# Kernel optimization log

Measured on AMD Instinct MI355X. Metric: run time of the kernel, lower is better.

## Reference

```python
import jax, jax.numpy as jnp
import numpy as np

I, H, NH, A = 128, 2048, 2, 4   # input_size, hidden_size, n_hidden, alpha_dim
K = 2 * A * A                   # per-position theta entries
B = 8192


def make_masks():
    # MADE sequential-ordering masks, identical to DART.create_masks
    inp = np.arange(I)
    degrees = [inp] + [np.arange(H) % (I - 1) for _ in range(NH + 1)] + [np.arange(I) - 1]
    masks = [(d1[:, None] >= d0[None, :]).astype(np.float32)
             for d0, d1 in zip(degrees[:-1], degrees[1:])]
    # last mask repeated per theta entry: repeat(1, K).view(-1, H) == row-repeat
    masks[-1] = np.repeat(masks[-1], K, axis=0)
    return [jnp.asarray(m) for m in masks]


def setup_inputs() -> dict:
    key = jax.random.key(0)
    ks = jax.random.split(key, 5)
    x = jax.random.normal(ks[0], (B, I), dtype=jnp.float32)

    def lin(k, out_dim, in_dim):
        kw, kb = jax.random.split(k)
        s = 1.0 / np.sqrt(in_dim)
        W = jax.random.uniform(kw, (out_dim, in_dim), minval=-s, maxval=s, dtype=jnp.float32)
        b = jax.random.uniform(kb, (out_dim,), minval=-s, maxval=s, dtype=jnp.float32)
        return W, b

    W0, b0 = lin(ks[1], H, I)
    W1, b1 = lin(ks[2], H, H)
    W2, b2 = lin(ks[3], H, H)
    W3, b3 = lin(ks[4], I * K, H)
    return dict(x=x, W0=W0, b0=b0, W1=W1, b1=b1, W2=W2, b2=b2, W3=W3, b3=b3)


def logexpmm(a, b):
    # log-domain matmul: out[..., i, j] = logsumexp_k(a[..., i, k] + b[..., k, j])
    return jax.nn.logsumexp(a[..., :, :, None] + b[..., None, :, :], axis=-2)


def reference(x, W0, b0, W1, b1, W2, b2, W3, b3):
    m = make_masks()
    h = jax.nn.relu(x @ (m[0] * W0).T + b0)
    h = jax.nn.relu(h @ (m[1] * W1).T + b1)
    h = jax.nn.relu(h @ (m[2] * W2).T + b2)
    theta = (h @ (m[3] * W3).T + b3).reshape(-1, I, 2, A, A)
    mu, alpha = theta[:, :, 0], theta[:, :, 1]  # (B, I, A, A)

    LOG2PI = float(np.log(2.0 * np.pi))
    xe = x[:, :, None, None]
    # Normal(mu, exp(alpha)).log_prob(x) - log(alpha_dim)
    logp = (-0.5 * ((xe - mu) * jnp.exp(-alpha)) ** 2
            - alpha - 0.5 * LOG2PI - jnp.log(jnp.float32(A)))

    first = logp[:, 0, 0:1]        # (B, 1, A)
    last = logp[:, -1, :, 0:1]     # (B, A, 1)
    inner = jnp.swapaxes(logp[:, 1:-1], 0, 1)  # (I-2, B, A, A)

    def step(carry, mtx):
        return logexpmm(carry, mtx), None

    prod, _ = jax.lax.scan(step, inner[0], inner[1:])
    return logexpmm(first, logexpmm(prod, last))  # (B, 1, 1)
```

## Files before the change

kernel.cpp:

```cpp
#include <hip/hip_runtime.h>
#include <hip/hip_bf16.h>
#include <cstdint>
#include <cstddef>

#define AS1 __attribute__((address_space(1)))
#define AS3 __attribute__((address_space(3)))

typedef __bf16 bf16x8  __attribute__((ext_vector_type(8)));
typedef float  floatx4 __attribute__((ext_vector_type(4)));

__device__ __forceinline__ void load_lds16(const void* g, void* l) {
    __builtin_amdgcn_global_load_lds((AS1 void*)g, (AS3 void*)l, 16, 0, 0);
}

__device__ __forceinline__ float fexp2(float x) { return __builtin_amdgcn_exp2f(x); }
__device__ __forceinline__ float flog2(float x) { return __builtin_amdgcn_logf(x); }

#define LOG2E 1.4426950408889634f
#define LN2   0.6931471805599453f
#define C0K   2.3052328943245633f

__device__ __forceinline__ float logp2(float xv, float mu, float al) {
    float e = fexp2(-al * LOG2E);
    float z = (xv - mu) * e;
    return (-0.5f * z * z - al - C0K) * LOG2E;
}
__device__ __forceinline__ float lse4(float a0, float a1, float a2, float a3) {
    float mx = fmaxf(fmaxf(a0, a1), fmaxf(a2, a3));
    return mx + flog2(fexp2(a0 - mx) + fexp2(a1 - mx) +
                      fexp2(a2 - mx) + fexp2(a3 - mx));
}
__device__ __forceinline__ void lmm4(const float* Aa, const float* Bb, float* D) {
#pragma unroll
    for (int r = 0; r < 4; ++r)
#pragma unroll
        for (int c = 0; c < 4; ++c)
            D[r * 4 + c] = lse4(Aa[r * 4 + 0] + Bb[0 * 4 + c],
                                Aa[r * 4 + 1] + Bb[1 * 4 + c],
                                Aa[r * 4 + 2] + Bb[2 * 4 + c],
                                Aa[r * 4 + 3] + Bb[3 * 4 + c]);
}

__device__ __forceinline__ int resp_s(int p) {
    return p < 272 ? p / 17 : 16 + ((p - 272) >> 4);
}
__device__ __forceinline__ int invp_s(int p) {
    if (p < 272) { int d = p / 17; int r = p - d * 17;
                   return r < 16 ? d + r * 127 : 2032 + d; }
    int d = 16 + ((p - 272) >> 4); int j = (p - 272) & 15;
    return d + j * 127;
}
__device__ __forceinline__ int cnt_le(int D) {
    return D < 16 ? (D + 1) * 17 : 272 + ((D - 15) << 4);
}

__global__ __launch_bounds__(256)
void prep_all(const float* __restrict__ x,  const float* __restrict__ W0,
              const float* __restrict__ W1, const float* __restrict__ W2,
              const float* __restrict__ W3,
              __bf16* __restrict__ xb,  __bf16* __restrict__ w0m,
              __bf16* __restrict__ w1m, __bf16* __restrict__ w2m,
              __bf16* __restrict__ w3m)
{
    __shared__ float lds[2048];
    const int blk = blockIdx.x;
    const int tid = threadIdx.x;
    const int t8  = tid * 8;

    if (blk < 640) {
        bf16x8 o;
        if (blk < 512) {
            size_t base = (size_t)blk * 2048 + t8;
            floatx4 a = *(const floatx4*)(x + base);
            floatx4 b = *(const floatx4*)(x + base + 4);
#pragma unroll
            for (int j = 0; j < 4; ++j) { o[j] = (__bf16)a[j]; o[4 + j] = (__bf16)b[j]; }
            *(bf16x8*)(xb + base) = o;
        } else {
            long idx = (long)(blk - 512) * 2048 + t8;
            int p_n = (int)(idx >> 7);
            int c   = (int)(idx & 127);
            int dg  = resp_s(p_n);
            const float* s = W0 + (long)invp_s(p_n) * 128 + c;
            floatx4 a = *(const floatx4*)s;
            floatx4 b = *(const floatx4*)(s + 4);
#pragma unroll
            for (int j = 0; j < 8; ++j) {
                float v = j < 4 ? a[j] : b[j - 4];
                o[j] = (__bf16)((dg >= c + j) ? v : 0.0f);
            }
            *(bf16x8*)(w0m + idx) = o;
        }
        return;
    }

    const float* srow; __bf16* drow; int deg_n; bool strict;
    if (blk < 2688) {
        int p_n = blk - 640;
        srow = W1 + (size_t)invp_s(p_n) * 2048; drow = w1m + (size_t)p_n * 2048;
        deg_n = resp_s(p_n); strict = false;
    } else if (blk < 4736) {
        int p_n = blk - 2688;
        srow = W2 + (size_t)invp_s(p_n) * 2048; drow = w2m + (size_t)p_n * 2048;
        deg_n = resp_s(p_n); strict = false;
    } else {
        int n = blk - 4736;
        srow = W3 + (size_t)n * 2048; drow = w3m + (size_t)n * 2048;
        deg_n = n >> 5; strict = true;
    }
    floatx4 a = *(const floatx4*)(srow + t8);
    floatx4 b = *(const floatx4*)(srow + t8 + 4);
    *(floatx4*)&lds[t8]     = a;
    *(floatx4*)&lds[t8 + 4] = b;
    __syncthreads();
    bf16x8 o;
#pragma unroll
    for (int j = 0; j < 8; ++j) {
        int p = t8 + j;
        float v = lds[invp_s(p)];
        int dg = resp_s(p);
        bool keep = strict ? (deg_n > dg) : (deg_n >= dg);
        o[j] = (__bf16)(keep ? v : 0.0f);
    }
    *(bf16x8*)(drow + t8) = o;
}

template <bool RELU, bool OBF16, bool TLAYOUT, bool PERMBIAS, int LMODE>
__global__ __launch_bounds__(256, 4)
void gemm_bt(const __bf16* __restrict__ A, const __bf16* __restrict__ Bw,
             const float* __restrict__ bias, void* __restrict__ Cout,
             int N, int K)
{
    __shared__ __align__(16) __bf16 lsA[128 * 64];
    __shared__ __align__(16) __bf16 lsB[128 * 64];
    const int tid  = threadIdx.x;
    const int wave = tid >> 6;
    const int lane = tid & 63;
    const int bm = blockIdx.x;
    const int bn = (gridDim.y - 1) - blockIdx.y;
    const int wm = wave >> 1, wn = wave & 1;

    const int r8 = lane >> 3;
    const int cb = (lane & 7) ^ r8;
    const __bf16* gsrc[8];
    __bf16* ldst[8];
#pragma unroll
    for (int t = 0; t < 8; ++t) {
        int j = wave * 8 + t;
        if (j < 16) {
            int row = bm * 128 + j * 8 + r8;
            gsrc[t] = A + (size_t)row * K + cb * 8;
            ldst[t] = lsA + j * 512;
        } else {
            int jj = j - 16;
            int row = bn * 128 + jj * 8 + r8;
            gsrc[t] = Bw + (size_t)row * K + cb * 8;
            ldst[t] = lsB + jj * 512;
        }
    }

    const int fr  = lane & 15;
    const int ks  = lane >> 4;
    const int sx  = fr & 7;
    const int sl0 = ((ks)     ^ sx) * 8;
    const int sl1 = ((4 + ks) ^ sx) * 8;
    const __bf16* arow[4];
    const __bf16* brow[4];
#pragma unroll
    for (int i = 0; i < 4; ++i) {
        arow[i] = lsA + (wm * 64 + i * 16 + fr) * 64;
        brow[i] = lsB + (wn * 64 + i * 16 + fr) * 64;
    }

    floatx4 acc[4][4];
    const floatx4 vzero = {0.f, 0.f, 0.f, 0.f};
#pragma unroll
    for (int mi = 0; mi < 4; ++mi)
#pragma unroll
        for (int ni = 0; ni < 4; ++ni) acc[mi][ni] = vzero;

    const int nk = K >> 6;
    int limit;
    if (LMODE == 0)      limit = (cnt_le(resp_s(bn * 128 + 127)) + 63) >> 6;
    else if (LMODE == 1) { int D = 4 * bn + 2; if (D > 126) D = 126;
                           limit = (cnt_le(D) + 63) >> 6; }
    else                 limit = (resp_s(bn * 128 + 127) + 64) >> 6;
    if (limit > nk) limit = nk;

    for (int it = 0; it < limit; ++it) {
        const int kt = it << 6;
        __syncthreads();
#pragma unroll
        for (int t = 0; t < 8; ++t)
            load_lds16((const void*)(gsrc[t] + kt), (void*)ldst[t]);
        __syncthreads();
        bf16x8 af[4], bf[4];
#pragma unroll
        for (int i = 0; i < 4; ++i) af[i] = *(const bf16x8*)(arow[i] + sl0);
#pragma unroll
        for (int i = 0; i < 4; ++i) bf[i] = *(const bf16x8*)(brow[i] + sl0);
#pragma unroll
        for (int mi = 0; mi < 4; ++mi)
#pragma unroll
            for (int ni = 0; ni < 4; ++ni)
                acc[mi][ni] = __builtin_amdgcn_mfma_f32_16x16x32_bf16(
                    af[mi], bf[ni], acc[mi][ni], 0, 0, 0);
#pragma unroll
        for (int i = 0; i < 4; ++i) af[i] = *(const bf16x8*)(arow[i] + sl1);
#pragma unroll
        for (int i = 0; i < 4; ++i) bf[i] = *(const bf16x8*)(brow[i] + sl1);
#pragma unroll
        for (int mi = 0; mi < 4; ++mi)
#pragma unroll
            for (int ni = 0; ni < 4; ++ni)
                acc[mi][ni] = __builtin_amdgcn_mfma_f32_16x16x32_bf16(
                    af[mi], bf[ni], acc[mi][ni], 0, 0, 0);
    }

    const int cn  = lane & 15;
    const int cr4 = (lane >> 4) * 4;
#pragma unroll
    for (int ni = 0; ni < 4; ++ni) {
        int col = bn * 128 + wn * 64 + ni * 16 + cn;
        float bv = bias[PERMBIAS ? invp_s(col) : col];
#pragma unroll
        for (int mi = 0; mi < 4; ++mi) {
            int row0 = bm * 128 + wm * 64 + mi * 16 + cr4;
#pragma unroll
            for (int q = 0; q < 4; ++q) {
                float v = acc[mi][ni][q] + bv;
                if (RELU) v = fmaxf(v, 0.f);
                if (TLAYOUT) {
                    size_t addr = (size_t)(bm * 2 + wm) * ((size_t)N * 64)
                                + (size_t)col * 64 + (mi * 16 + cr4 + q);
                    ((__bf16*)Cout)[addr] = (__bf16)v;
                } else if (OBF16) {
                    ((__bf16*)Cout)[(size_t)(row0 + q) * N + col] = (__bf16)v;
                } else {
                    ((float*)Cout)[(size_t)(row0 + q) * N + col] = v;
                }
            }
        }
    }
}

#define CFENCE() asm volatile("" ::: "memory")
#define BARX()  do { CFENCE(); __builtin_amdgcn_s_barrier(); CFENCE(); } while (0)
#define WVM2()  asm volatile("s_waitcnt vmcnt(2)" ::: "memory")
#define WVM0()  asm volatile("s_waitcnt vmcnt(0)" ::: "memory")
#define WLGK()  asm volatile("s_waitcnt lgkmcnt(0)" ::: "memory")

template <bool RELU, bool OBF16, bool TLAYOUT, bool PERMBIAS, int LMODE>
__global__ __launch_bounds__(512)
void gemm8p(const __bf16* __restrict__ A, const __bf16* __restrict__ Bw,
            const float* __restrict__ bias, void* __restrict__ Cout,
            int N, int K)
{
    __shared__ __align__(16) __bf16 ls[2 * 24576];
    const int tid  = threadIdx.x;
    const int wave = tid >> 6;
    const int lane = tid & 63;
    const int bm = blockIdx.x;
    const int bn = (gridDim.y - 1) - blockIdx.y;
    const int wm = wave >> 1, wn = wave & 1;

    const int l8 = lane >> 3;
    const int cb = (lane & 7) ^ l8;
    const __bf16* gA[2][2];  int dA[2][2];
    const __bf16* gB[2];     int dB[2];
#pragma unroll
    for (int h = 0; h < 2; ++h)
#pragma unroll
        for (int s = 0; s < 2; ++s) {
            int rt = h * 128 + wave * 16 + s * 8;
            gA[h][s] = A + (size_t)(bm * 256 + rt + l8) * K + cb * 8;
            dA[h][s] = rt * 64;
        }
#pragma unroll
    for (int s = 0; s < 2; ++s) {
        int rt = wave * 16 + s * 8;
        gB[s] = Bw + (size_t)(bn * 128 + rt + l8) * K + cb * 8;
        dB[s] = 16384 + rt * 64;
    }

#define STG_A(buf, kt) do { \
    load_lds16((const void*)(gA[0][0] + (kt)), (void*)(ls + (buf)*24576 + dA[0][0])); \
    load_lds16((const void*)(gA[0][1] + (kt)), (void*)(ls + (buf)*24576 + dA[0][1])); \
    load_lds16((const void*)(gA[1][0] + (kt)), (void*)(ls + (buf)*24576 + dA[1][0])); \
    load_lds16((const void*)(gA[1][1] + (kt)), (void*)(ls + (buf)*24576 + dA[1][1])); } while (0)
#define STG_B(buf, kt) do { \
    load_lds16((const void*)(gB[0] + (kt)), (void*)(ls + (buf)*24576 + dB[0])); \
    load_lds16((const void*)(gB[1] + (kt)), (void*)(ls + (buf)*24576 + dB[1])); } while (0)

    const int fr  = lane & 15;
    const int ks  = lane >> 4;
    const int sx  = fr & 7;
    const int sl0 = ((ks)     ^ sx) * 8;
    const int sl1 = ((4 + ks) ^ sx) * 8;
    int aoff[4], boff[4];
#pragma unroll
    for (int i = 0; i < 4; ++i) {
        aoff[i] = (wm * 64 + i * 16 + fr) * 64;
        boff[i] = 16384 + (wn * 64 + i * 16 + fr) * 64;
    }

    floatx4 acc[4][4];
    const floatx4 vzero = {0.f, 0.f, 0.f, 0.f};
#pragma unroll
    for (int mi = 0; mi < 4; ++mi)
#pragma unroll
        for (int ni = 0; ni < 4; ++ni) acc[mi][ni] = vzero;

    bf16x8 bfr[4][2], afr[2][2];

#define DSRD_B(buf) do { \
    _Pragma("unroll") \
    for (int ni = 0; ni < 4; ++ni) { \
        bfr[ni][0] = *(const bf16x8*)(ls + (buf)*24576 + boff[ni] + sl0); \
        bfr[ni][1] = *(const bf16x8*)(ls + (buf)*24576 + boff[ni] + sl1); } } while (0)
#define DSRD_A(buf, q) do { \
    _Pragma("unroll") \
    for (int j = 0; j < 2; ++j) { \
        afr[j][0] = *(const bf16x8*)(ls + (buf)*24576 + aoff[2*(q)+j] + sl0); \
        afr[j][1] = *(const bf16x8*)(ls + (buf)*24576 + aoff[2*(q)+j] + sl1); } } while (0)
#define MFMA16(q) do { \
    __builtin_amdgcn_s_setprio(1); \
    _Pragma("unroll") \
    for (int j = 0; j < 2; ++j) \
    _Pragma("unroll") \
    for (int ni = 0; ni < 4; ++ni) { \
        acc[2*(q)+j][ni] = __builtin_amdgcn_mfma_f32_16x16x32_bf16( \
            afr[j][0], bfr[ni][0], acc[2*(q)+j][ni], 0, 0, 0); \
        acc[2*(q)+j][ni] = __builtin_amdgcn_mfma_f32_16x16x32_bf16( \
            afr[j][1], bfr[ni][1], acc[2*(q)+j][ni], 0, 0, 0); } \
    __builtin_amdgcn_s_setprio(0); } while (0)

    const int nk = K >> 6;
    int limit;
    if (LMODE == 0)      limit = (cnt_le(resp_s(bn * 128 + 127)) + 63) >> 6;
    else if (LMODE == 1) { int D = 4 * bn + 2; if (D > 126) D = 126;
                           limit = (cnt_le(D) + 63) >> 6; }
    else                 limit = (resp_s(bn * 128 + 127) + 64) >> 6;
    if (limit > nk) limit = nk;
    const int NT = limit;

    STG_B(0, 0);
    STG_A(0, 0);
    if (NT > 1) { STG_B(1, 64); WVM2(); } else { WVM0(); }
    BARX();

    for (int t = 0; ; t += 2) {
        const int kt1 = (t + 1) << 6, kt2 = (t + 2) << 6, kt3 = (t + 3) << 6;
        const bool has1 = t + 1 < NT, has2 = t + 2 < NT, has3 = t + 3 < NT;

        DSRD_B(0);
        DSRD_A(0, 0);
        if (has1) STG_A(1, kt1);
        BARX(); WLGK();
        MFMA16(0);
        BARX();

        DSRD_A(0, 1);
        if (has2) STG_B(0, kt2);
        BARX(); WLGK();
        MFMA16(1);
        if (!has1) break;
        if (has2) WVM2(); else WVM0();
        BARX();

        DSRD_B(1);
        DSRD_A(1, 0);
        if (has2) STG_A(0, kt2);
        BARX(); WLGK();
        MFMA16(0);
        BARX();

        DSRD_A(1, 1);
        if (has3) STG_B(1, kt3);
        BARX(); WLGK();
        MFMA16(1);
        if (!has2) break;
        if (has3) WVM2(); else WVM0();
        BARX();
    }

    const int cn  = lane & 15;
    const int cr4 = (lane >> 4) * 4;
#pragma unroll
    for (int ni = 0; ni < 4; ++ni) {
        int col = bn * 128 + wn * 64 + ni * 16 + cn;
        float bv = bias[PERMBIAS ? invp_s(col) : col];
#pragma unroll
        for (int mi = 0; mi < 4; ++mi) {
            int row0 = bm * 256 + wm * 64 + mi * 16 + cr4;
#pragma unroll
            for (int q = 0; q < 4; ++q) {
                float v = acc[mi][ni][q] + bv;
                if (RELU) v = fmaxf(v, 0.f);
                if (TLAYOUT) {
                    size_t addr = (size_t)(bm * 4 + wm) * ((size_t)N * 64)
                                + (size_t)col * 64 + (mi * 16 + cr4 + q);
                    ((__bf16*)Cout)[addr] = (__bf16)v;
                } else if (OBF16) {
                    ((__bf16*)Cout)[(size_t)(row0 + q) * N + col] = (__bf16)v;
                } else {
                    ((float*)Cout)[(size_t)(row0 + q) * N + col] = v;
                }
            }
        }
    }
#undef STG_A
#undef STG_B
#undef DSRD_B
#undef DSRD_A
#undef MFMA16
}

__global__ __launch_bounds__(448)
void chain_all(const __bf16* __restrict__ th2,
               const float* __restrict__ x,
               float* __restrict__ out)
{
    __shared__ float xs[32 * 129];
    __shared__ float Pl[32 * 238];
    const int tid = threadIdx.x;
    const int blk = blockIdx.x;

    for (int idx = tid; idx < 4096; idx += 448) {
        int bl = idx >> 7, i = idx & 127;
        xs[bl * 129 + i] = x[(size_t)blk * 4096 + idx];
    }
    __syncthreads();

    const int s  = tid >> 5;
    const int bl = tid & 31;
    const int b64 = (blk & 1) * 32 + bl;
    const __bf16* tb = th2 + (size_t)(blk >> 1) * (4096 * 64) + b64;

    {
        const int i0 = 1 + s * 9;
        const __bf16* tp = tb + (size_t)i0 * 32 * 64;
        float M[4][4];
#pragma unroll
        for (int r = 0; r < 4; ++r)
#pragma unroll
            for (int c = 0; c < 4; ++c) M[r][c] = (r == c) ? 0.f : -1e30f;

        for (int ii = 0; ii < 9; ++ii) {
            float mu[16], al[16];
#pragma unroll
            for (int j = 0; j < 16; ++j) mu[j] = (float)tp[(size_t)j * 64];
#pragma unroll
            for (int j = 0; j < 16; ++j) al[j] = (float)tp[(size_t)(16 + j) * 64];
            float xv = xs[bl * 129 + i0 + ii];
            tp += 2048;
            float lp[16];
#pragma unroll
            for (int j = 0; j < 16; ++j) lp[j] = logp2(xv, mu[j], al[j]);
            float Mn[4][4];
#pragma unroll
            for (int r = 0; r < 4; ++r)
#pragma unroll
                for (int c = 0; c < 4; ++c)
                    Mn[r][c] = lse4(M[r][0] + lp[0 + c], M[r][1] + lp[4 + c],
                                    M[r][2] + lp[8 + c], M[r][3] + lp[12 + c]);
#pragma unroll
            for (int r = 0; r < 4; ++r)
#pragma unroll
                for (int c = 0; c < 4; ++c) M[r][c] = Mn[r][c];
        }
        float* pb = Pl + bl * 238 + s * 17;
#pragma unroll
        for (int r = 0; r < 4; ++r)
#pragma unroll
            for (int c = 0; c < 4; ++c) pb[r * 4 + c] = M[r][c];
    }
    __syncthreads();

    float Q[16];
    if (tid < 224) {
        const float* base = Pl + bl * 238;
        lmm4(base + (2 * s) * 17, base + (2 * s + 1) * 17, Q);
    }
    __syncthreads();
    if (tid < 224) {
        float* dst = Pl + bl * 238 + s * 17;
#pragma unroll
        for (int e = 0; e < 16; ++e) dst[e] = Q[e];
    }
    __syncthreads();

    if (tid < 32) {
        const float* base = Pl + tid * 238;
        float M[16], T[16];
#pragma unroll
        for (int e = 0; e < 16; ++e) M[e] = base[e];
#pragma unroll
        for (int j = 1; j < 7; ++j) {
            lmm4(M, base + j * 17, T);
#pragma unroll
            for (int e = 0; e < 16; ++e) M[e] = T[e];
        }
        const int bb64 = (blk & 1) * 32 + tid;
        const __bf16* tbb = th2 + (size_t)(blk >> 1) * (4096 * 64) + bb64;
        float x0 = xs[tid * 129 + 0];
        float xl = xs[tid * 129 + 127];
        float last[4], t4[4], f4[4];
#pragma unroll
        for (int c = 0; c < 4; ++c)
            last[c] = logp2(xl, (float)tbb[(size_t)(4064 + c * 4) * 64],
                                (float)tbb[(size_t)(4064 + 16 + c * 4) * 64]);
#pragma unroll
        for (int r = 0; r < 4; ++r)
            t4[r] = lse4(M[r * 4 + 0] + last[0], M[r * 4 + 1] + last[1],
                         M[r * 4 + 2] + last[2], M[r * 4 + 3] + last[3]);
#pragma unroll
        for (int r = 0; r < 4; ++r)
            f4[r] = logp2(x0, (float)tbb[(size_t)r * 64],
                              (float)tbb[(size_t)(16 + r) * 64]);
        out[blk * 32 + tid] = LN2 * lse4(f4[0] + t4[0], f4[1] + t4[1],
                                         f4[2] + t4[2], f4[3] + t4[3]);
    }
}

extern "C" void kernel_launch(void* const* d_in, const int* in_sizes, int n_in,
                              void* d_out, int out_size, void* d_ws, size_t ws_size,
                              hipStream_t stream)
{
    (void)in_sizes; (void)n_in; (void)out_size; (void)ws_size;
    const float* x  = (const float*)d_in[0];
    const float* W0 = (const float*)d_in[1];
    const float* b0 = (const float*)d_in[2];
    const float* W1 = (const float*)d_in[3];
    const float* b1 = (const float*)d_in[4];
    const float* W2 = (const float*)d_in[5];
    const float* b2 = (const float*)d_in[6];
    const float* W3 = (const float*)d_in[7];
    const float* b3 = (const float*)d_in[8];

    char* ws = (char*)d_ws;
    const size_t MB = 1024 * 1024;
    __bf16* h2  = (__bf16*)(ws + 0);
    __bf16* xb  = (__bf16*)(ws + 32 * MB);
    __bf16* w0m = (__bf16*)(ws + 34 * MB);
    __bf16* w1m = (__bf16*)(ws + 35 * MB);
    __bf16* w2m = (__bf16*)(ws + 43 * MB);
    __bf16* th  = (__bf16*)(ws + 0);
    __bf16* w3m = (__bf16*)(ws + 64 * MB);
    __bf16* h1  = (__bf16*)(ws + 80 * MB);
    __bf16* h3  = h1;

    prep_all<<<8832, 256, 0, stream>>>(x, W0, W1, W2, W3, xb, w0m, w1m, w2m, w3m);

    gemm_bt<true, true, false, true, 2><<<dim3(64, 16), 256, 0, stream>>>(
        xb, w0m, b0, h1, 2048, 128);
    gemm8p<true, true, false, true, 0><<<dim3(32, 16), 512, 0, stream>>>(
        h1, w1m, b1, h2, 2048, 2048);
    gemm8p<true, true, false, true, 0><<<dim3(32, 16), 512, 0, stream>>>(
        h2, w2m, b2, h3, 2048, 2048);
    gemm8p<false, false, true, false, 1><<<dim3(32, 32), 512, 0, stream>>>(
        h3, w3m, b3, th, 4096, 2048);

    chain_all<<<256, 448, 0, stream>>>(th, x, (float*)d_out);
}
```

Measured before the change: 322.0 us.

## Use 256x256-tile GEMM kernel for final masked projection layer

Adds a new GEMM kernel with 256x256 output tiles per 512-thread block, using double-buffered global-to-LDS loads, finer interleaving of LDS reads with MFMA in half-tiles, and partial vmcnt waits. The final W3 projection now runs on it with half as many blocks. Larger tiles raise arithmetic intensity and cut global traffic per FLOP, but they also mean fewer blocks and more register and LDS pressure, which lowers occupancy. They also make the masked-K limit per tile coarser.

```diff
diff --git a/kernel.cpp b/kernel.cpp
--- a/kernel.cpp
+++ b/kernel.cpp
@@ -246,6 +246,7 @@
 
 #define CFENCE() asm volatile("" ::: "memory")
 #define BARX()  do { CFENCE(); __builtin_amdgcn_s_barrier(); CFENCE(); } while (0)
+#define WVM6()  asm volatile("s_waitcnt vmcnt(6)" ::: "memory")
 #define WVM2()  asm volatile("s_waitcnt vmcnt(2)" ::: "memory")
 #define WVM0()  asm volatile("s_waitcnt vmcnt(0)" ::: "memory")
 #define WLGK()  asm volatile("s_waitcnt lgkmcnt(0)" ::: "memory")
@@ -416,6 +417,194 @@
 #undef MFMA16
 }
 
+template <bool RELU, bool OBF16, bool TLAYOUT, bool PERMBIAS, int LMODE>
+__global__ __launch_bounds__(512)
+void gemm256(const __bf16* __restrict__ A, const __bf16* __restrict__ Bw,
+             const float* __restrict__ bias, void* __restrict__ Cout,
+             int N, int K)
+{
+    __shared__ __align__(16) __bf16 ls[2 * 32768];
+    const int tid  = threadIdx.x;
+    const int wave = tid >> 6;
+    const int lane = tid & 63;
+    const int bm = blockIdx.x;
+    const int bn = (gridDim.y - 1) - blockIdx.y;
+    const int wm = wave >> 2, wn = wave & 3;
+
+    const int l8 = lane >> 3;
+    const int cb = (lane & 7) ^ l8;
+    const __bf16* gA[2][2]; int lA[2][2];
+    const __bf16* gB[2][2]; int lB[2][2];
+#pragma unroll
+    for (int h = 0; h < 2; ++h)
+#pragma unroll
+        for (int c = 0; c < 2; ++c) {
+            int rA = ((wave & 4) ? 128 : 0) + h * 64 + (wave & 3) * 16 + c * 8;
+            gA[h][c] = A + (size_t)(bm * 256 + rA + l8) * K + cb * 8;
+            lA[h][c] = (rA + l8) * 64 + (lane & 7) * 8;
+            int rB = (wave >> 1) * 64 + h * 32 + (wave & 1) * 16 + c * 8;
+            gB[h][c] = Bw + (size_t)(bn * 256 + rB + l8) * K + cb * 8;
+            lB[h][c] = 16384 + (rB + l8) * 64 + (lane & 7) * 8;
+        }
+
+#define STG_AU(h, buf, kt) do { \
+    load_lds16((const void*)(gA[h][0] + (kt)), (void*)(ls + (buf)*32768 + lA[h][0])); \
+    load_lds16((const void*)(gA[h][1] + (kt)), (void*)(ls + (buf)*32768 + lA[h][1])); } while (0)
+#define STG_BU(h, buf, kt) do { \
+    load_lds16((const void*)(gB[h][0] + (kt)), (void*)(ls + (buf)*32768 + lB[h][0])); \
+    load_lds16((const void*)(gB[h][1] + (kt)), (void*)(ls + (buf)*32768 + lB[h][1])); } while (0)
+
+    const int fr  = lane & 15;
+    const int ks  = lane >> 4;
+    const int sx  = fr & 7;
+    const int sl0 = ((ks)     ^ sx) * 8;
+    const int sl1 = ((4 + ks) ^ sx) * 8;
+    int aof[2][4], bof[2][2];
+#pragma unroll
+    for (int h = 0; h < 2; ++h) {
+#pragma unroll
+        for (int m = 0; m < 4; ++m)
+            aof[h][m] = (wm * 128 + h * 64 + m * 16 + fr) * 64;
+#pragma unroll
+        for (int n = 0; n < 2; ++n)
+            bof[h][n] = 16384 + (wn * 64 + h * 32 + n * 16 + fr) * 64;
+    }
+
+    bf16x8 af[4][2], b0[2][2], b1[2][2];
+    floatx4 acc[8][4];
+    const floatx4 vzero = {0.f, 0.f, 0.f, 0.f};
+#pragma unroll
+    for (int mi = 0; mi < 8; ++mi)
+#pragma unroll
+        for (int ni = 0; ni < 4; ++ni) acc[mi][ni] = vzero;
+
+#define DSRD_A2(buf, mh) do { _Pragma("unroll") \
+    for (int m = 0; m < 4; ++m) { \
+        af[m][0] = *(const bf16x8*)(ls + (buf)*32768 + aof[mh][m] + sl0); \
+        af[m][1] = *(const bf16x8*)(ls + (buf)*32768 + aof[mh][m] + sl1); } } while (0)
+#define DSRD_B0(buf) do { _Pragma("unroll") \
+    for (int n = 0; n < 2; ++n) { \
+        b0[n][0] = *(const bf16x8*)(ls + (buf)*32768 + bof[0][n] + sl0); \
+        b0[n][1] = *(const bf16x8*)(ls + (buf)*32768 + bof[0][n] + sl1); } } while (0)
+#define DSRD_B1(buf) do { _Pragma("unroll") \
+    for (int n = 0; n < 2; ++n) { \
+        b1[n][0] = *(const bf16x8*)(ls + (buf)*32768 + bof[1][n] + sl0); \
+        b1[n][1] = *(const bf16x8*)(ls + (buf)*32768 + bof[1][n] + sl1); } } while (0)
+#define MF16(mh, BF, nh) do { \
+    __builtin_amdgcn_s_setprio(1); \
+    _Pragma("unroll") \
+    for (int m = 0; m < 4; ++m) \
+    _Pragma("unroll") \
+    for (int n = 0; n < 2; ++n) { \
+        acc[(mh)*4+m][(nh)*2+n] = __builtin_amdgcn_mfma_f32_16x16x32_bf16( \
+            af[m][0], BF[n][0], acc[(mh)*4+m][(nh)*2+n], 0, 0, 0); \
+        acc[(mh)*4+m][(nh)*2+n] = __builtin_amdgcn_mfma_f32_16x16x32_bf16( \
+            af[m][1], BF[n][1], acc[(mh)*4+m][(nh)*2+n], 0, 0, 0); } \
+    __builtin_amdgcn_s_setprio(0); } while (0)
+
+    const int nk = K >> 6;
+    int limit;
+    if (LMODE == 0)      limit = (cnt_le(resp_s(bn * 256 + 255)) + 63) >> 6;
+    else if (LMODE == 1) { int D = 8 * bn + 6; if (D > 126) D = 126;
+                           limit = (cnt_le(D) + 63) >> 6; }
+    else                 limit = (resp_s(bn * 256 + 255) + 64) >> 6;
+    if (limit > nk) limit = nk;
+    const int NT = limit;
+
+    STG_AU(0, 0, 0); STG_BU(0, 0, 0); STG_BU(1, 0, 0); STG_AU(1, 0, 0);
+    if (NT > 1) { STG_AU(0, 1, 64); STG_BU(0, 1, 64); STG_BU(1, 1, 64); WVM6(); }
+    else        { WVM0(); }
+    BARX();
+
+    int t = 0;
+    for (; t + 1 < NT; t += 2) {
+        const int kt1 = (t + 1) << 6, kt2 = (t + 2) << 6, kt3 = (t + 3) << 6;
+        const bool st2 = (t + 2 < NT), st3 = (t + 3 < NT);
+
+        DSRD_A2(0, 0); DSRD_B0(0);
+        STG_AU(1, 1, kt1);
+        BARX(); WLGK();
+        MF16(0, b0, 0);
+        BARX();
+        DSRD_B1(0);
+        if (st2) STG_AU(0, 0, kt2);
+        BARX(); WLGK();
+        MF16(0, b1, 1);
+        BARX();
+        DSRD_A2(0, 1);
+        if (st2) STG_BU(0, 0, kt2);
+        BARX(); WLGK();
+        MF16(1, b1, 1);
+        BARX();
+        if (st2) STG_BU(1, 0, kt2);
+        BARX();
+        MF16(1, b0, 0);
+        if (st2) WVM6(); else WVM0();
+        BARX();
+        DSRD_A2(1, 0); DSRD_B0(1);
+        if (st2) STG_AU(1, 0, kt2);
+        BARX(); WLGK();
+        MF16(0, b0, 0);
+        BARX();
+        DSRD_B1(1);
+        if (st3) STG_AU(0, 1, kt3);
+        BARX(); WLGK();
+        MF16(0, b1, 1);
+        BARX();
+        DSRD_A2(1, 1);
+        if (st3) STG_BU(0, 1, kt3);
+        BARX(); WLGK();
+        MF16(1, b1, 1);
+        BARX();
+        if (st3) STG_BU(1, 1, kt3);
+        BARX();
+        MF16(1, b0, 0);
+        if (st3) WVM6(); else WVM0();
+        BARX();
+    }
+    if (t < NT) {
+        DSRD_A2(0, 0); DSRD_B0(0); WLGK();
+        MF16(0, b0, 0);
+        DSRD_B1(0); WLGK();
+        MF16(0, b1, 1);
+        DSRD_A2(0, 1); WLGK();
+        MF16(1, b1, 1);
+        MF16(1, b0, 0);
+    }
+
+    const int cn  = lane & 15;
+    const int cr4 = (lane >> 4) * 4;
+#pragma unroll
+    for (int ni = 0; ni < 4; ++ni) {
+        int col = bn * 256 + wn * 64 + ni * 16 + cn;
+        float bv = bias[PERMBIAS ? invp_s(col) : col];
+#pragma unroll
+        for (int mi = 0; mi < 8; ++mi) {
+            int row0 = bm * 256 + wm * 128 + mi * 16 + cr4;
+#pragma unroll
+            for (int q = 0; q < 4; ++q) {
+                float v = acc[mi][ni][q] + bv;
+                if (RELU) v = fmaxf(v, 0.f);
+                if (TLAYOUT) {
+                    size_t addr = (size_t)(bm * 4 + wm * 2 + (mi >> 2)) * ((size_t)N * 64)
+                                + (size_t)col * 64 + ((mi & 3) * 16 + cr4 + q);
+                    ((__bf16*)Cout)[addr] = (__bf16)v;
+                } else if (OBF16) {
+                    ((__bf16*)Cout)[(size_t)(row0 + q) * N + col] = (__bf16)v;
+                } else {
+                    ((float*)Cout)[(size_t)(row0 + q) * N + col] = v;
+                }
+            }
+        }
+    }
+#undef STG_AU
+#undef STG_BU
+#undef DSRD_A2
+#undef DSRD_B0
+#undef DSRD_B1
+#undef MF16
+}
+
 __global__ __launch_bounds__(448)
 void chain_all(const __bf16* __restrict__ th2,
                const float* __restrict__ x,
@@ -558,7 +747,7 @@
         h1, w1m, b1, h2, 2048, 2048);
     gemm8p<true, true, false, true, 0><<<dim3(32, 16), 512, 0, stream>>>(
         h2, w2m, b2, h3, 2048, 2048);
-    gemm8p<false, false, true, false, 1><<<dim3(32, 32), 512, 0, stream>>>(
+    gemm256<false, false, true, false, 1><<<dim3(32, 16), 512, 0, stream>>>(
         h3, w3m, b3, th, 4096, 2048);
 
     chain_all<<<256, 448, 0, stream>>>(th, x, (float*)d_out);
```

New measurement: 367.2 us. 14.0% more time.
